# Kernel tuning notes

Hardware: AMD Instinct MI355X
Metric: run time of the kernel (lower is better)

Reference implementation:

```python
import jax, jax.numpy as jnp
import numpy as np

N, C, H, W = 64, 3, 345, 456


def _gs_linspace(n):
    # torch affine_grid (align_corners=False) coordinate vector:
    # symmetric construction: forward linspace for i < n/2, mirrored for i >= n/2
    i = jnp.arange(n)
    step = 2.0 / n
    start = -(1.0 - 1.0 / n)
    fwd = i.astype(jnp.float32) * step + start
    bwd = -start - (n - 1 - i).astype(jnp.float32) * step
    return jnp.where(i < n / 2.0, fwd, bwd)


def setup_inputs() -> dict:
    key = jax.random.key(0)
    k1, k2 = jax.random.split(key)
    x = jax.random.normal(k1, (N, C, H, W), dtype=jnp.float32)
    eye = jnp.array([[1.0, 0.0, 0.0], [0.0, 1.0, 0.0]], dtype=jnp.float32)
    theta = jnp.tile(eye[None], (N, 1, 1)) + 0.1 * jax.random.normal(k2, (N, 2, 3), dtype=jnp.float32)
    return {"x": x, "theta": theta}


def _grid_sample_bilinear_zeros(x, theta):
    n, c, h, w = x.shape
    xs = _gs_linspace(w)                       # [W]
    ys = _gs_linspace(h)                       # [H]
    base = jnp.stack(
        [jnp.broadcast_to(xs[None, :], (h, w)),
         jnp.broadcast_to(ys[:, None], (h, w)),
         jnp.ones((h, w), jnp.float32)], axis=-1)          # [H,W,3]
    grid = jnp.einsum('hwk,nok->nhwo', base, theta)         # [N,H,W,2]
    # unnormalize (align_corners=False): ix = gx*W/2 + (W-1)/2
    ix = grid[..., 0] * (w / 2.0) + (w - 1) / 2.0
    iy = grid[..., 1] * (h / 2.0) + (h - 1) / 2.0
    x0 = jnp.floor(ix)
    y0 = jnp.floor(iy)
    x1 = x0 + 1.0
    y1 = y0 + 1.0

    def corner(xc, yc, wt):
        valid = (xc >= 0) & (xc < w) & (yc >= 0) & (yc < h)
        xi = jnp.where(valid, xc, 0.0).astype(jnp.int32)    # [N,H,W]
        yi = jnp.where(valid, yc, 0.0).astype(jnp.int32)
        wts = jnp.where(valid, wt, 0.0)
        # gather per batch: img[C,H,W], yi/xi [H,W] -> [C,H,W]
        vals = jax.vmap(lambda img, yy, xx: img[:, yy, xx])(x, yi, xi)  # [N,C,H,W]
        return vals * wts[:, None]

    out = (corner(x0, y0, (x1 - ix) * (y1 - iy))
           + corner(x1, y0, (ix - x0) * (y1 - iy))
           + corner(x0, y1, (x1 - ix) * (iy - y0))
           + corner(x1, y1, (ix - x0) * (iy - y0)))
    return out


def reference(x, theta):
    return _grid_sample_bilinear_zeros(x, theta)
```

## Files before the change

kernel.cpp:

```cpp
#include <hip/hip_runtime.h>

constexpr int N_ = 64, C_ = 3, H_ = 345, W_ = 456;
constexpr int HW_ = H_ * W_;

constexpr int TW = 32, TH = 16;
constexpr int TX = 15, TY = 22;
constexpr int TILES = TX * TY;
constexpr int CCAP = 52;
constexpr int RCAP = 28;
constexpr int CH_STRIDE = RCAP * CCAP;
constexpr int SLOTS = (CCAP / 4) * RCAP;

typedef __attribute__((ext_vector_type(2))) float f32x2;

__device__ __forceinline__ void make_win(
    int w0, int h0, float Ax, float Bx, float Cx, float Ay, float By, float Cy,
    int& xa_out, int& ylo_out)
{
    float ws = (float)w0, we = (float)min(w0 + TW - 1, W_ - 1);
    float hs = (float)h0, he = (float)min(h0 + TH - 1, H_ - 1);
    float xw0 = ws * Ax, xw1 = we * Ax;
    float xh0 = hs * Bx, xh1 = he * Bx;
    float minix = Cx + fminf(xw0, xw1) + fminf(xh0, xh1);
    float maxix = Cx + fmaxf(xw0, xw1) + fmaxf(xh0, xh1);
    float yw0 = ws * Ay, yw1 = we * Ay;
    float yh0 = hs * By, yh1 = he * By;
    float miniy = Cy + fminf(yw0, yw1) + fminf(yh0, yh1);
    float maxiy = Cy + fmaxf(yw0, yw1) + fmaxf(yh0, yh1);

    int x_lo = (int)floorf(minix) - 1, x_hi = (int)floorf(maxix) + 2;
    int y_lo = (int)floorf(miniy) - 1, y_hi = (int)floorf(maxiy) + 2;

    int xa = x_lo & ~3;
    int cols4 = (x_hi - xa + 4) >> 2;
    if (cols4 > CCAP / 4) xa += ((cols4 - CCAP / 4) >> 1) << 2;
    int rows = y_hi - y_lo + 1;
    if (rows > RCAP) y_lo += (rows - RCAP) >> 1;

    xa   = max(0, min(xa,   W_ - CCAP));
    y_lo = max(0, min(y_lo, H_ - RCAP));
    xa_out = xa; ylo_out = y_lo;
}

__global__ __launch_bounds__(256) void gs_tiled(
    const float* __restrict__ x,
    const float* __restrict__ theta,
    float* __restrict__ out)
{
    __shared__ float lds[3 * CH_STRIDE];

    int b    = blockIdx.x;
    int xcd  = b & 7;
    int i    = b >> 3;
    int bg   = i / TILES;
    int tile = i - bg * TILES;
    int n    = xcd + 8 * bg;

    int ty = tile / TX;
    int tx = tile - ty * TX;
    int w0 = tx * TW, h0 = ty * TH;

    const float* t = theta + n * 6;
    float t00 = t[0], t01 = t[1], t02 = t[2];
    float t10 = t[3], t11 = t[4], t12 = t[5];

    const float halfW = 0.5f * (float)W_, cW = 0.5f * (float)(W_ - 1);
    const float halfH = 0.5f * (float)H_, cH = 0.5f * (float)(H_ - 1);
    const float startx = -(1.0f - 1.0f / (float)W_);
    const float starty = -(1.0f - 1.0f / (float)H_);

    float Ax = t00;
    float Bx = t01 * ((float)W_ / (float)H_);
    float Cx = fmaf(startx, t00, fmaf(starty, t01, t02)) * halfW + cW;
    float Ay = t10 * ((float)H_ / (float)W_);
    float By = t11;
    float Cy = fmaf(startx, t10, fmaf(starty, t11, t12)) * halfH + cH;

    const float* xn = x + (size_t)n * 3 * HW_;
    float* on = out + (size_t)n * 3 * HW_;

    int tid = threadIdx.x;

    int cxa, cylo;
    make_win(w0, h0, Ax, Bx, Cx, Ay, By, Cy, cxa, cylo);

    {
        int s1 = tid;
        int r1 = s1 / 13, j1 = s1 - 13 * r1;
        const float* g1 = xn + (size_t)(cylo + r1) * W_ + cxa + 4 * j1;
        float4 a0 = *(const float4*)(g1);
        float4 a1 = *(const float4*)(g1 + HW_);
        float4 a2 = *(const float4*)(g1 + 2 * HW_);
        float* d1 = lds + 4 * s1;
        *(float4*)(d1)                 = a0;
        *(float4*)(d1 + CH_STRIDE)     = a1;
        *(float4*)(d1 + 2 * CH_STRIDE) = a2;

        int s2 = tid + 256;
        if (s2 < SLOTS) {
            int r2 = s2 / 13, j2 = s2 - 13 * r2;
            const float* g2 = xn + (size_t)(cylo + r2) * W_ + cxa + 4 * j2;
            float4 b0 = *(const float4*)(g2);
            float4 b1 = *(const float4*)(g2 + HW_);
            float4 b2 = *(const float4*)(g2 + 2 * HW_);
            float* d2 = lds + 4 * s2;
            *(float4*)(d2)                 = b0;
            *(float4*)(d2 + CH_STRIDE)     = b1;
            *(float4*)(d2 + 2 * CH_STRIDE) = b2;
        }
    }
    __syncthreads();

    int tw = (tid & 15) * 2, th = tid >> 4;
    int w = w0 + tw, h = h0 + th;
    if (w >= W_ || h >= H_) return;

    float fw = (float)w, fh = (float)h;
    float hx  = fmaf(fh, Bx, Cx), hy = fmaf(fh, By, Cy);
    float ixA = fmaf(fw, Ax, hx), iyA = fmaf(fw, Ay, hy);
    float ixB = ixA + Ax,         iyB = iyA + Ay;

    float xfA = floorf(ixA), yfA = floorf(iyA);
    float fxA = ixA - xfA,   fyA = iyA - yfA;
    int   XA  = (int)xfA,    YA  = (int)yfA;

    float xfB = floorf(ixB), yfB = floorf(iyB);
    float fxB = ixB - xfB,   fyB = iyB - yfB;
    int   XB  = (int)xfB,    YB  = (int)yfB;

    int lcA = XA - cxa, lrA = YA - cylo;
    int lcB = XB - cxa, lrB = YB - cylo;
    bool inA = (unsigned)lcA < (unsigned)(CCAP - 1) && (unsigned)lrA < (unsigned)(RCAP - 1);
    bool inB = (unsigned)lcB < (unsigned)(CCAP - 1) && (unsigned)lrB < (unsigned)(RCAP - 1);

    size_t o = (size_t)h * W_ + w;

    if (__builtin_expect(inA & inB, 1)) {
        const float* pA = lds + lrA * CCAP + lcA;
        const float* pB = lds + lrB * CCAP + lcB;
        f32x2 FX = {fxA, fxB};
        f32x2 FY = {fyA, fyB};

        {
            f32x2 P00 = {pA[0],        pB[0]};
            f32x2 P10 = {pA[1],        pB[1]};
            f32x2 P01 = {pA[CCAP],     pB[CCAP]};
            f32x2 P11 = {pA[CCAP + 1], pB[CCAP + 1]};
            f32x2 top = (P10 - P00) * FX + P00;
            f32x2 bot = (P11 - P01) * FX + P01;
            f32x2 v   = (bot - top) * FY + top;
            *(float2*)(on + o) = make_float2(v.x, v.y);
        }
        {
            f32x2 P00 = {pA[CH_STRIDE],            pB[CH_STRIDE]};
            f32x2 P10 = {pA[CH_STRIDE + 1],        pB[CH_STRIDE + 1]};
            f32x2 P01 = {pA[CH_STRIDE + CCAP],     pB[CH_STRIDE + CCAP]};
            f32x2 P11 = {pA[CH_STRIDE + CCAP + 1], pB[CH_STRIDE + CCAP + 1]};
            f32x2 top = (P10 - P00) * FX + P00;
            f32x2 bot = (P11 - P01) * FX + P01;
            f32x2 v   = (bot - top) * FY + top;
            *(float2*)(on + o + HW_) = make_float2(v.x, v.y);
        }
        {
            f32x2 P00 = {pA[2 * CH_STRIDE],            pB[2 * CH_STRIDE]};
            f32x2 P10 = {pA[2 * CH_STRIDE + 1],        pB[2 * CH_STRIDE + 1]};
            f32x2 P01 = {pA[2 * CH_STRIDE + CCAP],     pB[2 * CH_STRIDE + CCAP]};
            f32x2 P11 = {pA[2 * CH_STRIDE + CCAP + 1], pB[2 * CH_STRIDE + CCAP + 1]};
            f32x2 top = (P10 - P00) * FX + P00;
            f32x2 bot = (P11 - P01) * FX + P01;
            f32x2 v   = (bot - top) * FY + top;
            *(float2*)(on + o + 2 * HW_) = make_float2(v.x, v.y);
        }
    } else {
        float gxA = 1.0f - fxA, gyA = 1.0f - fyA;
        float gxB = 1.0f - fxB, gyB = 1.0f - fyB;
        float wA00 = gxA * gyA, wA10 = fxA * gyA, wA01 = gxA * fyA, wA11 = fxA * fyA;
        float wB00 = gxB * gyB, wB10 = fxB * gyB, wB01 = gxB * fyB, wB11 = fxB * fyB;
        float vA0 = 0, vA1 = 0, vA2 = 0, vB0 = 0, vB1 = 0, vB2 = 0;
#define CORNG(xi, yi, wt, d0, d1, d2)                                         \
        if ((unsigned)(xi) < (unsigned)W_ && (unsigned)(yi) < (unsigned)H_) { \
            int off = (yi) * W_ + (xi);                                       \
            d0 += xn[off] * (wt);                                             \
            d1 += xn[HW_ + off] * (wt);                                       \
            d2 += xn[2 * HW_ + off] * (wt);                                   \
        }
        CORNG(XA,     YA,     wA00, vA0, vA1, vA2)
        CORNG(XA + 1, YA,     wA10, vA0, vA1, vA2)
        CORNG(XA,     YA + 1, wA01, vA0, vA1, vA2)
        CORNG(XA + 1, YA + 1, wA11, vA0, vA1, vA2)
        CORNG(XB,     YB,     wB00, vB0, vB1, vB2)
        CORNG(XB + 1, YB,     wB10, vB0, vB1, vB2)
        CORNG(XB,     YB + 1, wB01, vB0, vB1, vB2)
        CORNG(XB + 1, YB + 1, wB11, vB0, vB1, vB2)
#undef CORNG
        *(float2*)(on + o)           = make_float2(vA0, vB0);
        *(float2*)(on + o + HW_)     = make_float2(vA1, vB1);
        *(float2*)(on + o + 2 * HW_) = make_float2(vA2, vB2);
    }
}

extern "C" void kernel_launch(void* const* d_in, const int* in_sizes, int n_in,
                              void* d_out, int out_size, void* d_ws, size_t ws_size,
                              hipStream_t stream) {
    const float* x     = (const float*)d_in[0];
    const float* theta = (const float*)d_in[1];
    float* out = (float*)d_out;

    int blocks = N_ * TILES;
    gs_tiled<<<blocks, 256, 0, stream>>>(x, theta, out);
}
```

Before: 44.31 us.

## Enlarge tiles to 64x16 with 1024-thread blocks, one pixel per thread

Widens each output tile from 32x16 to 64x16 pixels and launches 1024 threads per block, so each thread now produces one pixel instead of two. The shared-memory halo window grows to 96x40 and is staged in a single pass. Larger tiles cut the redundant halo loading per output pixel and halve the block count. In exchange each block uses more LDS, which may limit occupancy, and output stores become scalar rather than float2.

```diff
diff --git a/kernel.cpp b/kernel.cpp
--- a/kernel.cpp
+++ b/kernel.cpp
@@ -3,15 +3,13 @@
 constexpr int N_ = 64, C_ = 3, H_ = 345, W_ = 456;
 constexpr int HW_ = H_ * W_;
 
-constexpr int TW = 32, TH = 16;
-constexpr int TX = 15, TY = 22;
+constexpr int TW = 64, TH = 16;
+constexpr int TX = 8, TY = 22;
 constexpr int TILES = TX * TY;
-constexpr int CCAP = 52;
-constexpr int RCAP = 28;
+constexpr int CCAP = 96;
+constexpr int RCAP = 40;
 constexpr int CH_STRIDE = RCAP * CCAP;
 constexpr int SLOTS = (CCAP / 4) * RCAP;
-
-typedef __attribute__((ext_vector_type(2))) float f32x2;
 
 __device__ __forceinline__ void make_win(
     int w0, int h0, float Ax, float Bx, float Cx, float Ay, float By, float Cy,
@@ -42,7 +40,7 @@
     xa_out = xa; ylo_out = y_lo;
 }
 
-__global__ __launch_bounds__(256) void gs_tiled(
+__global__ __launch_bounds__(1024) void gs_tiled(
     const float* __restrict__ x,
     const float* __restrict__ theta,
     float* __restrict__ out)
@@ -84,118 +82,76 @@
     int cxa, cylo;
     make_win(w0, h0, Ax, Bx, Cx, Ay, By, Cy, cxa, cylo);
 
-    {
-        int s1 = tid;
-        int r1 = s1 / 13, j1 = s1 - 13 * r1;
+    if (tid < SLOTS) {
+        int r1 = tid / 24, j1 = tid - 24 * r1;
         const float* g1 = xn + (size_t)(cylo + r1) * W_ + cxa + 4 * j1;
         float4 a0 = *(const float4*)(g1);
         float4 a1 = *(const float4*)(g1 + HW_);
         float4 a2 = *(const float4*)(g1 + 2 * HW_);
-        float* d1 = lds + 4 * s1;
+        float* d1 = lds + 4 * tid;
         *(float4*)(d1)                 = a0;
         *(float4*)(d1 + CH_STRIDE)     = a1;
         *(float4*)(d1 + 2 * CH_STRIDE) = a2;
-
-        int s2 = tid + 256;
-        if (s2 < SLOTS) {
-            int r2 = s2 / 13, j2 = s2 - 13 * r2;
-            const float* g2 = xn + (size_t)(cylo + r2) * W_ + cxa + 4 * j2;
-            float4 b0 = *(const float4*)(g2);
-            float4 b1 = *(const float4*)(g2 + HW_);
-            float4 b2 = *(const float4*)(g2 + 2 * HW_);
-            float* d2 = lds + 4 * s2;
-            *(float4*)(d2)                 = b0;
-            *(float4*)(d2 + CH_STRIDE)     = b1;
-            *(float4*)(d2 + 2 * CH_STRIDE) = b2;
-        }
     }
     __syncthreads();
 
-    int tw = (tid & 15) * 2, th = tid >> 4;
-    int w = w0 + tw, h = h0 + th;
+    int w = w0 + (tid & 63), h = h0 + (tid >> 6);
     if (w >= W_ || h >= H_) return;
 
     float fw = (float)w, fh = (float)h;
-    float hx  = fmaf(fh, Bx, Cx), hy = fmaf(fh, By, Cy);
-    float ixA = fmaf(fw, Ax, hx), iyA = fmaf(fw, Ay, hy);
-    float ixB = ixA + Ax,         iyB = iyA + Ay;
+    float ix = fmaf(fw, Ax, fmaf(fh, Bx, Cx));
+    float iy = fmaf(fw, Ay, fmaf(fh, By, Cy));
 
-    float xfA = floorf(ixA), yfA = floorf(iyA);
-    float fxA = ixA - xfA,   fyA = iyA - yfA;
-    int   XA  = (int)xfA,    YA  = (int)yfA;
+    float xf = floorf(ix), yf = floorf(iy);
+    float fx = ix - xf,    fy = iy - yf;
+    int   X0 = (int)xf,    Y0 = (int)yf;
 
-    float xfB = floorf(ixB), yfB = floorf(iyB);
-    float fxB = ixB - xfB,   fyB = iyB - yfB;
-    int   XB  = (int)xfB,    YB  = (int)yfB;
-
-    int lcA = XA - cxa, lrA = YA - cylo;
-    int lcB = XB - cxa, lrB = YB - cylo;
-    bool inA = (unsigned)lcA < (unsigned)(CCAP - 1) && (unsigned)lrA < (unsigned)(RCAP - 1);
-    bool inB = (unsigned)lcB < (unsigned)(CCAP - 1) && (unsigned)lrB < (unsigned)(RCAP - 1);
+    int lc = X0 - cxa, lr = Y0 - cylo;
+    bool in = (unsigned)lc < (unsigned)(CCAP - 1) && (unsigned)lr < (unsigned)(RCAP - 1);
 
     size_t o = (size_t)h * W_ + w;
 
-    if (__builtin_expect(inA & inB, 1)) {
-        const float* pA = lds + lrA * CCAP + lcA;
-        const float* pB = lds + lrB * CCAP + lcB;
-        f32x2 FX = {fxA, fxB};
-        f32x2 FY = {fyA, fyB};
-
+    if (__builtin_expect(in, 1)) {
+        const float* p = lds + lr * CCAP + lc;
         {
-            f32x2 P00 = {pA[0],        pB[0]};
-            f32x2 P10 = {pA[1],        pB[1]};
-            f32x2 P01 = {pA[CCAP],     pB[CCAP]};
-            f32x2 P11 = {pA[CCAP + 1], pB[CCAP + 1]};
-            f32x2 top = (P10 - P00) * FX + P00;
-            f32x2 bot = (P11 - P01) * FX + P01;
-            f32x2 v   = (bot - top) * FY + top;
-            *(float2*)(on + o) = make_float2(v.x, v.y);
+            float p00 = p[0], p10 = p[1], p01 = p[CCAP], p11 = p[CCAP + 1];
+            float tp = fmaf(fx, p10 - p00, p00);
+            float bt = fmaf(fx, p11 - p01, p01);
+            on[o] = fmaf(fy, bt - tp, tp);
         }
         {
-            f32x2 P00 = {pA[CH_STRIDE],            pB[CH_STRIDE]};
-            f32x2 P10 = {pA[CH_STRIDE + 1],        pB[CH_STRIDE + 1]};
-            f32x2 P01 = {pA[CH_STRIDE + CCAP],     pB[CH_STRIDE + CCAP]};
-            f32x2 P11 = {pA[CH_STRIDE + CCAP + 1], pB[CH_STRIDE + CCAP + 1]};
-            f32x2 top = (P10 - P00) * FX + P00;
-            f32x2 bot = (P11 - P01) * FX + P01;
-            f32x2 v   = (bot - top) * FY + top;
-            *(float2*)(on + o + HW_) = make_float2(v.x, v.y);
+            float p00 = p[CH_STRIDE],        p10 = p[CH_STRIDE + 1];
+            float p01 = p[CH_STRIDE + CCAP], p11 = p[CH_STRIDE + CCAP + 1];
+            float tp = fmaf(fx, p10 - p00, p00);
+            float bt = fmaf(fx, p11 - p01, p01);
+            on[o + HW_] = fmaf(fy, bt - tp, tp);
         }
         {
-            f32x2 P00 = {pA[2 * CH_STRIDE],            pB[2 * CH_STRIDE]};
-            f32x2 P10 = {pA[2 * CH_STRIDE + 1],        pB[2 * CH_STRIDE + 1]};
-            f32x2 P01 = {pA[2 * CH_STRIDE + CCAP],     pB[2 * CH_STRIDE + CCAP]};
-            f32x2 P11 = {pA[2 * CH_STRIDE + CCAP + 1], pB[2 * CH_STRIDE + CCAP + 1]};
-            f32x2 top = (P10 - P00) * FX + P00;
-            f32x2 bot = (P11 - P01) * FX + P01;
-            f32x2 v   = (bot - top) * FY + top;
-            *(float2*)(on + o + 2 * HW_) = make_float2(v.x, v.y);
+            float p00 = p[2 * CH_STRIDE],        p10 = p[2 * CH_STRIDE + 1];
+            float p01 = p[2 * CH_STRIDE + CCAP], p11 = p[2 * CH_STRIDE + CCAP + 1];
+            float tp = fmaf(fx, p10 - p00, p00);
+            float bt = fmaf(fx, p11 - p01, p01);
+            on[o + 2 * HW_] = fmaf(fy, bt - tp, tp);
         }
     } else {
-        float gxA = 1.0f - fxA, gyA = 1.0f - fyA;
-        float gxB = 1.0f - fxB, gyB = 1.0f - fyB;
-        float wA00 = gxA * gyA, wA10 = fxA * gyA, wA01 = gxA * fyA, wA11 = fxA * fyA;
-        float wB00 = gxB * gyB, wB10 = fxB * gyB, wB01 = gxB * fyB, wB11 = fxB * fyB;
-        float vA0 = 0, vA1 = 0, vA2 = 0, vB0 = 0, vB1 = 0, vB2 = 0;
-#define CORNG(xi, yi, wt, d0, d1, d2)                                         \
+        float gx1 = 1.0f - fx, gy1 = 1.0f - fy;
+        float w00 = gx1 * gy1, w10 = fx * gy1, w01 = gx1 * fy, w11 = fx * fy;
+        float a0 = 0.0f, a1 = 0.0f, a2 = 0.0f;
+#define CORNG(xi, yi, wt)                                                     \
         if ((unsigned)(xi) < (unsigned)W_ && (unsigned)(yi) < (unsigned)H_) { \
             int off = (yi) * W_ + (xi);                                       \
-            d0 += xn[off] * (wt);                                             \
-            d1 += xn[HW_ + off] * (wt);                                       \
-            d2 += xn[2 * HW_ + off] * (wt);                                   \
+            a0 += xn[off] * (wt);                                             \
+            a1 += xn[HW_ + off] * (wt);                                       \
+            a2 += xn[2 * HW_ + off] * (wt);                                   \
         }
-        CORNG(XA,     YA,     wA00, vA0, vA1, vA2)
-        CORNG(XA + 1, YA,     wA10, vA0, vA1, vA2)
-        CORNG(XA,     YA + 1, wA01, vA0, vA1, vA2)
-        CORNG(XA + 1, YA + 1, wA11, vA0, vA1, vA2)
-        CORNG(XB,     YB,     wB00, vB0, vB1, vB2)
-        CORNG(XB + 1, YB,     wB10, vB0, vB1, vB2)
-        CORNG(XB,     YB + 1, wB01, vB0, vB1, vB2)
-        CORNG(XB + 1, YB + 1, wB11, vB0, vB1, vB2)
+        CORNG(X0,     Y0,     w00)
+        CORNG(X0 + 1, Y0,     w10)
+        CORNG(X0,     Y0 + 1, w01)
+        CORNG(X0 + 1, Y0 + 1, w11)
 #undef CORNG
-        *(float2*)(on + o)           = make_float2(vA0, vB0);
-        *(float2*)(on + o + HW_)     = make_float2(vA1, vB1);
-        *(float2*)(on + o + 2 * HW_) = make_float2(vA2, vB2);
+        on[o]           = a0;
+        on[o + HW_]     = a1;
+        on[o + 2 * HW_] = a2;
     }
 }
 
@@ -207,5 +163,5 @@
     float* out = (float*)d_out;
 
     int blocks = N_ * TILES;
-    gs_tiled<<<blocks, 256, 0, stream>>>(x, theta, out);
+    gs_tiled<<<blocks, 1024, 0, stream>>>(x, theta, out);
 }
```

Result: slower. 55.27 us (+24.7%).
